# Kernel tuning notes

Hardware: AMD Instinct MI355X
Metric: run time of the kernel (lower is better)

Reference implementation:

```python
import jax, jax.numpy as jnp
import numpy as np


def _ste_round(r):
    # straight-through round
    return r + jax.lax.stop_gradient(jnp.round(r) - r)


def quant_sym(x, s, qn, qp):
    # symmetric LSQ-style fake-quant: clamp(round(x/s)) * s
    r = jnp.clip(x / s, qn, qp)
    return _ste_round(r) * s


def quant_asym(x, s, beta, qn, qp):
    # asymmetric fake-quant with learnable zero-point beta
    r = jnp.clip((x - beta) / s, qn, qp)
    return _ste_round(r) * s + beta


def quant_weight_statsq(w, n_bits=8):
    # statsq: per-output-channel scale from weight statistics
    qp = 2 ** (n_bits - 1) - 1          # 127
    qn = -(2 ** (n_bits - 1))           # -128
    s = 2.0 * jnp.mean(jnp.abs(w), axis=1, keepdims=True) / jnp.sqrt(float(qp))
    return quant_sym(w, s, qn, qp)


def setup_inputs() -> dict:
    key = jax.random.key(0)
    ks = jax.random.split(key, 8)
    B, N, C, H = 4, 4096, 1024, 4096
    x = jax.random.normal(ks[0], (B, N, C), dtype=jnp.float32)
    w1 = jax.random.normal(ks[1], (H, C), dtype=jnp.float32) * (1.0 / np.sqrt(C))
    b1 = jax.random.normal(ks[2], (H,), dtype=jnp.float32) * 0.01
    w2 = jax.random.normal(ks[3], (C, H), dtype=jnp.float32) * (1.0 / np.sqrt(H))
    b2 = jax.random.normal(ks[4], (C,), dtype=jnp.float32) * 0.01
    # learnable LSQ activation scales (per input channel), kept positive
    s_a1 = 0.05 + 0.05 * jax.random.uniform(ks[5], (C,), dtype=jnp.float32)
    s_a2 = 0.02 + 0.02 * jax.random.uniform(ks[6], (H,), dtype=jnp.float32)
    beta2 = jnp.zeros((H,), dtype=jnp.float32)
    return {"x": x, "w1": w1, "b1": b1, "w2": w2, "b2": b2,
            "s_a1": s_a1, "s_a2": s_a2, "beta2": beta2}


def reference(x, w1, b1, w2, b2, s_a1, s_a2, beta2):
    # fc1: symmetric 8-bit LSQ on input, statsq 8-bit on weight
    xq = quant_sym(x, s_a1, -128, 127)
    wq1 = quant_weight_statsq(w1)
    h = jnp.einsum('bnc,hc->bnh', xq, wq1) + b1
    h = jax.nn.gelu(h, approximate=False)  # nn.GELU default (exact erf)
    # drop1 = identity in eval
    # fc2: asymmetric 8-bit LSQ on (non-negative-skewed) activations
    hq = quant_asym(h, s_a2, beta2, 0, 255)
    wq2 = quant_weight_statsq(w2)
    out = jnp.einsum('bnh,ch->bnc', hq, wq2) + b2
    # drop2 = identity in eval
    return out
```

## Files before the change

kernel.cpp:

```cpp
#include <hip/hip_runtime.h>
#include <cstdint>
#include <cstddef>

typedef __attribute__((ext_vector_type(8))) short short8;
typedef __attribute__((ext_vector_type(4))) float f32x4;
typedef __attribute__((ext_vector_type(4))) unsigned short ushort4_t;

__device__ __forceinline__ unsigned short f2bf(float f) {
  unsigned u = __float_as_uint(f);
  u += 0x7FFFu + ((u >> 16) & 1u);
  return (unsigned short)(u >> 16);
}

__device__ __forceinline__ void gload_lds16(const void* g, void* lds) {
  __builtin_amdgcn_global_load_lds((const __attribute__((address_space(1))) void*)g,
                                   (__attribute__((address_space(3))) void*)lds,
                                   16, 0, 0);
}

__device__ __forceinline__ float erf_fast(float v) {
  float x = fabsf(v);
  float t = __builtin_amdgcn_rcpf(fmaf(0.3275911f, x, 1.0f));
  float p = fmaf(1.061405429f, t, -1.453152027f);
  p = fmaf(p, t, 1.421413741f);
  p = fmaf(p, t, -0.284496736f);
  p = fmaf(p, t, 0.254829592f);
  p = p * t;
  float e = fmaf(-p, __expf(-x * x), 1.0f);
  unsigned s = __float_as_uint(v) & 0x80000000u;
  return __uint_as_float(__float_as_uint(e) | s);
}

__global__ void quant_x_kernel(const float4* __restrict__ x, const float* __restrict__ s_a1,
                               ushort4_t* __restrict__ xq, int n4, int c4mask) {
  const int stride = gridDim.x * blockDim.x;
  for (int i = blockIdx.x * blockDim.x + threadIdx.x; i < n4; i += stride) {
    float4 v = x[i];
    int c = (i & c4mask) << 2;
    float vv[4] = {v.x, v.y, v.z, v.w};
    ushort4_t o;
#pragma unroll
    for (int j = 0; j < 4; ++j) {
      float s = s_a1[c + j];
      float r = vv[j] / s;
      r = fminf(fmaxf(r, -128.f), 127.f);
      o[j] = f2bf(rintf(r) * s);
    }
    xq[i] = o;
  }
}

__global__ void quant_w_kernel(const float* __restrict__ w, unsigned short* __restrict__ wq,
                               int cols) {
  const int row = blockIdx.x;
  const float* wr = w + (size_t)row * cols;
  float part = 0.f;
  for (int j = threadIdx.x; j < cols; j += blockDim.x) part += fabsf(wr[j]);
#pragma unroll
  for (int o = 32; o > 0; o >>= 1) part += __shfl_down(part, o, 64);
  __shared__ float wsum[4];
  if ((threadIdx.x & 63) == 0) wsum[threadIdx.x >> 6] = part;
  __syncthreads();
  float mean = (wsum[0] + wsum[1] + wsum[2] + wsum[3]) / (float)cols;
  float s = 2.f * mean / sqrtf(127.f);
  unsigned short* wqr = wq + (size_t)row * cols;
  for (int j = threadIdx.x; j < cols; j += blockDim.x) {
    float r = wr[j] / s;
    r = fminf(fmaxf(r, -128.f), 127.f);
    wqr[j] = f2bf(rintf(r) * s);
  }
}

#define BAR() __builtin_amdgcn_s_barrier()
#define SB() __builtin_amdgcn_sched_barrier(0)
#define LGKM(n) { asm volatile("s_waitcnt lgkmcnt(" #n ")" ::: "memory"); SB(); }
#define VMC0() { asm volatile("s_waitcnt vmcnt(0)" ::: "memory"); SB(); }
#define PRIO1() __builtin_amdgcn_s_setprio(1)
#define PRIO0() __builtin_amdgcn_s_setprio(0)

#define STG(gbase, ldsbuf, h, kt) { \
  _Pragma("unroll") for (int i_ = 0; i_ < 2; ++i_) { \
    const int rb_ = (h) * 128 + (w * 2 + i_) * 8; \
    gload_lds16((gbase) + (size_t)rb_ * K + (size_t)(kt) * 64, (void*)((ldsbuf) + rb_ * 64)); } }

#define LDA_(dst, buf, mh) { \
  _Pragma("unroll") for (int mi_ = 0; mi_ < 4; ++mi_) { \
    dst[mi_][0] = *(const short8*)((buf) + aBase + (mh) * 4096 + mi_ * 1024 + ck0); \
    dst[mi_][1] = *(const short8*)((buf) + aBase + (mh) * 4096 + mi_ * 1024 + ck1); } }

#define LDB_(dst, buf, nh) { \
  _Pragma("unroll") for (int ni_ = 0; ni_ < 2; ++ni_) { \
    dst[ni_][0] = *(const short8*)((buf) + bBase + (nh) * 2048 + ni_ * 1024 + ck0); \
    dst[ni_][1] = *(const short8*)((buf) + bBase + (nh) * 2048 + ni_ * 1024 + ck1); } }

#define MMQ(aR, bR, mh, nh) { \
  _Pragma("unroll") for (int kk_ = 0; kk_ < 2; ++kk_) \
  _Pragma("unroll") for (int mi_ = 0; mi_ < 4; ++mi_) \
  _Pragma("unroll") for (int ni_ = 0; ni_ < 2; ++ni_) \
    acc[(mh) * 4 + mi_][(nh) * 2 + ni_] = __builtin_amdgcn_mfma_f32_16x16x32_bf16( \
        aR[mi_][kk_], bR[ni_][kk_], acc[(mh) * 4 + mi_][(nh) * 2 + ni_], 0, 0, 0); }

template <int EPI>
__global__ __launch_bounds__(512, 2) void gemm_bt_pl(
    const unsigned short* __restrict__ A, const unsigned short* __restrict__ B,
    const float* __restrict__ bias, const float* __restrict__ s2,
    const float* __restrict__ beta, unsigned short* __restrict__ Cq,
    float* __restrict__ Cf, int N, int K)
{
  __shared__ __align__(16) unsigned short As0[256 * 64];
  __shared__ __align__(16) unsigned short As1[256 * 64];
  __shared__ __align__(16) unsigned short Bs0[256 * 64];
  __shared__ __align__(16) unsigned short Bs1[256 * 64];

  const int tid = threadIdx.x;
  const int w = tid >> 6, ll = tid & 63;
  const int wr = w >> 2, wc = w & 3;
  const long bm = (long)blockIdx.x * 256;
  const long bn = (long)blockIdx.y * 256;

  const int srow = ll >> 3;
  const int scol = ((ll & 7) ^ srow) << 3;
  const unsigned short* Agl = A + ((size_t)bm + srow) * K + scol;
  const unsigned short* Bgl = B + ((size_t)bn + srow) * K + scol;

  const int lhi = ll >> 4, llo = ll & 15, l7 = ll & 7;
  const int ck0 = ((0 * 4 + lhi) ^ l7) * 8;
  const int ck1 = ((1 * 4 + lhi) ^ l7) * 8;
  const int aBase = (wr * 128 + llo) * 64;
  const int bBase = (wc * 64 + llo) * 64;

  f32x4 acc[8][4] = {};
  short8 a0[4][2], a1[4][2], b0[2][2], b1[2][2];

  const int nkt = K >> 6;

  STG(Agl, As0, 0, 0); STG(Agl, As0, 1, 0);
  STG(Bgl, Bs0, 0, 0); STG(Bgl, Bs0, 1, 0);
  STG(Agl, As1, 0, 1); STG(Agl, As1, 1, 1);
  STG(Bgl, Bs1, 0, 1); STG(Bgl, Bs1, 1, 1);
  asm volatile("s_waitcnt vmcnt(8)" ::: "memory"); SB();
  BAR();
  LDA_(a0, As0, 0);
  LDB_(b0, Bs0, 0);

  for (int t = 0; t < nkt; ++t) {
    unsigned short* Asb = (t & 1) ? As1 : As0;
    unsigned short* Bsb = (t & 1) ? Bs1 : Bs0;
    unsigned short* Asn = (t & 1) ? As0 : As1;
    unsigned short* Bsn = (t & 1) ? Bs0 : Bs1;
    const bool i1 = (t + 1 < nkt), i2 = (t + 2 < nkt);

    LDB_(b1, Bsb, 1);
    LGKM(4);
    PRIO1(); MMQ(a0, b0, 0, 0); PRIO0();
    LDA_(a1, Asb, 1);
    LGKM(8);
    PRIO1(); MMQ(a0, b1, 0, 1); PRIO0();
    LGKM(0);
    PRIO1(); MMQ(a1, b0, 1, 0); PRIO0();
    VMC0();
    BAR();
    if (i2) {
      STG(Agl, Asb, 0, t + 2); STG(Agl, Asb, 1, t + 2);
      STG(Bgl, Bsb, 0, t + 2); STG(Bgl, Bsb, 1, t + 2);
    }
    if (i1) {
      LDA_(a0, Asn, 0);
      LDB_(b0, Bsn, 0);
    }
    PRIO1(); MMQ(a1, b1, 1, 1); PRIO0();
  }

  const int lr = lhi;
  const int lc = llo;
#pragma unroll
  for (int NI = 0; NI < 4; ++NI) {
    const long col = bn + wc * 64 + NI * 16 + lc;
    const float bv = bias[col];
    float sv = 1.f, bev = 0.f, inv = 1.f;
    if (EPI == 0) { sv = s2[col]; bev = beta[col]; inv = 1.0f / sv; }
#pragma unroll
    for (int MI = 0; MI < 8; ++MI) {
#pragma unroll
      for (int r = 0; r < 4; ++r) {
        const size_t rowg = (size_t)(bm + wr * 128 + MI * 16 + lr * 4 + r);
        float v = acc[MI][NI][r] + bv;
        if (EPI == 0) {
          float g = 0.5f * v * (1.f + erf_fast(v * 0.70710678118654752f));
          float rr = (g - bev) * inv;
          rr = fminf(fmaxf(rr, 0.f), 255.f);
          Cq[rowg * N + col] = f2bf(fmaf(rintf(rr), sv, bev));
        } else {
          Cf[rowg * N + col] = v;
        }
      }
    }
  }
}

extern "C" void kernel_launch(void* const* d_in, const int* in_sizes, int n_in,
                              void* d_out, int out_size, void* d_ws, size_t ws_size,
                              hipStream_t stream) {
  const float* x     = (const float*)d_in[0];
  const float* w1    = (const float*)d_in[1];
  const float* b1    = (const float*)d_in[2];
  const float* w2    = (const float*)d_in[3];
  const float* b2    = (const float*)d_in[4];
  const float* s_a1  = (const float*)d_in[5];
  const float* s_a2  = (const float*)d_in[6];
  const float* beta2 = (const float*)d_in[7];
  float* out = (float*)d_out;

  const int C = 1024, H = 4096;
  const int M = in_sizes[0] / C;

  unsigned short* xq  = (unsigned short*)d_ws;
  unsigned short* wq1 = xq  + (size_t)M * C;
  unsigned short* wq2 = wq1 + (size_t)H * C;
  unsigned short* hq  = wq2 + (size_t)C * H;

  quant_x_kernel<<<2048, 256, 0, stream>>>((const float4*)x, s_a1, (ushort4_t*)xq,
                                           M * C / 4, C / 4 - 1);
  quant_w_kernel<<<H, 256, 0, stream>>>(w1, wq1, C);
  quant_w_kernel<<<C, 256, 0, stream>>>(w2, wq2, H);

  dim3 g1(M / 256, H / 256);
  gemm_bt_pl<0><<<g1, 512, 0, stream>>>(xq, wq1, b1, s_a2, beta2, hq, nullptr, H, C);
  dim3 g2(M / 256, C / 256);
  gemm_bt_pl<1><<<g2, 512, 0, stream>>>(hq, wq2, b2, nullptr, nullptr, nullptr, out, C, H);
}
```

Measured before the change: 367.0 us.

## Unroll GEMM main loop by two with reordered LDS loads and MFMA ordering

Restructures the GEMM K-loop to process two k-tiles per iteration with fixed buffer addresses. Fragment loads are interleaved in a different order so MFMA quadrants reuse already-loaded A/B fragments, which aims to hide more LDS latency. The epilogue also hoists per-column bias and scale loads and reorders the stores by row. This assumes nkt is even, which holds for K=1024 and K=4096, and it increases code size.

```diff
diff --git a/kernel.cpp b/kernel.cpp
--- a/kernel.cpp
+++ b/kernel.cpp
@@ -101,7 +101,7 @@
         aR[mi_][kk_], bR[ni_][kk_], acc[(mh) * 4 + mi_][(nh) * 2 + ni_], 0, 0, 0); }
 
 template <int EPI>
-__global__ __launch_bounds__(512, 2) void gemm_bt_pl(
+__global__ __launch_bounds__(512, 2) void gemm_bt_gc(
     const unsigned short* __restrict__ A, const unsigned short* __restrict__ B,
     const float* __restrict__ bias, const float* __restrict__ s2,
     const float* __restrict__ beta, unsigned short* __restrict__ Cq,
@@ -130,7 +130,7 @@
   const int bBase = (wc * 64 + llo) * 64;
 
   f32x4 acc[8][4] = {};
-  short8 a0[4][2], a1[4][2], b0[2][2], b1[2][2];
+  short8 pa0[4][2], pa1[4][2], pb0[2][2], pb1[2][2];
 
   const int nkt = K >> 6;
 
@@ -139,59 +139,77 @@
   STG(Agl, As1, 0, 1); STG(Agl, As1, 1, 1);
   STG(Bgl, Bs1, 0, 1); STG(Bgl, Bs1, 1, 1);
   asm volatile("s_waitcnt vmcnt(8)" ::: "memory"); SB();
-  BAR();
-  LDA_(a0, As0, 0);
-  LDB_(b0, Bs0, 0);
-
-  for (int t = 0; t < nkt; ++t) {
-    unsigned short* Asb = (t & 1) ? As1 : As0;
-    unsigned short* Bsb = (t & 1) ? Bs1 : Bs0;
-    unsigned short* Asn = (t & 1) ? As0 : As1;
-    unsigned short* Bsn = (t & 1) ? Bs0 : Bs1;
-    const bool i1 = (t + 1 < nkt), i2 = (t + 2 < nkt);
-
-    LDB_(b1, Bsb, 1);
-    LGKM(4);
-    PRIO1(); MMQ(a0, b0, 0, 0); PRIO0();
-    LDA_(a1, Asb, 1);
-    LGKM(8);
-    PRIO1(); MMQ(a0, b1, 0, 1); PRIO0();
-    LGKM(0);
-    PRIO1(); MMQ(a1, b0, 1, 0); PRIO0();
-    VMC0();
-    BAR();
-    if (i2) {
-      STG(Agl, Asb, 0, t + 2); STG(Agl, Asb, 1, t + 2);
-      STG(Bgl, Bsb, 0, t + 2); STG(Bgl, Bsb, 1, t + 2);
-    }
-    if (i1) {
-      LDA_(a0, Asn, 0);
-      LDB_(b0, Bsn, 0);
-    }
-    PRIO1(); MMQ(a1, b1, 1, 1); PRIO0();
+  BAR(); SB();
+  LDB_(pb0, Bs0, 0);
+  LDA_(pa0, As0, 0);
+
+  for (int t = 0; t < nkt; t += 2) {
+    {
+      const bool s2a = (t + 2 < nkt);
+      LDA_(pa1, As0, 1);
+      LGKM(8);
+      PRIO1(); MMQ(pa0, pb0, 0, 0); PRIO0();
+      LDB_(pb1, Bs0, 1);
+      LGKM(4);
+      PRIO1(); MMQ(pa1, pb0, 1, 0); PRIO0();
+      LGKM(0);
+      VMC0();
+      BAR(); SB();
+      if (s2a) { STG(Agl, As0, 0, t + 2); STG(Agl, As0, 1, t + 2);
+                 STG(Bgl, Bs0, 0, t + 2); STG(Bgl, Bs0, 1, t + 2); }
+      LDB_(pb0, Bs1, 0);
+      PRIO1(); MMQ(pa1, pb1, 1, 1); PRIO0();
+      LDA_(pa1, As1, 1);
+      PRIO1(); MMQ(pa0, pb1, 0, 1); PRIO0();
+    }
+    {
+      const int to = t + 1;
+      const bool cont = (to + 1 < nkt);
+      const bool s3 = (to + 2 < nkt);
+      LDA_(pa0, As1, 0);
+      LGKM(8);
+      PRIO1(); MMQ(pa1, pb0, 1, 0); PRIO0();
+      LDB_(pb1, Bs1, 1);
+      LGKM(4);
+      PRIO1(); MMQ(pa0, pb0, 0, 0); PRIO0();
+      LGKM(0);
+      VMC0();
+      BAR(); SB();
+      if (s3) { STG(Agl, As1, 0, to + 2); STG(Agl, As1, 1, to + 2);
+                STG(Bgl, Bs1, 0, to + 2); STG(Bgl, Bs1, 1, to + 2); }
+      if (cont) LDB_(pb0, Bs0, 0);
+      PRIO1(); MMQ(pa0, pb1, 0, 1); PRIO0();
+      if (cont) LDA_(pa0, As0, 0);
+      PRIO1(); MMQ(pa1, pb1, 1, 1); PRIO0();
+    }
   }
 
   const int lr = lhi;
   const int lc = llo;
+  float bv[4], sv[4], bev[4], inv[4];
 #pragma unroll
   for (int NI = 0; NI < 4; ++NI) {
     const long col = bn + wc * 64 + NI * 16 + lc;
-    const float bv = bias[col];
-    float sv = 1.f, bev = 0.f, inv = 1.f;
-    if (EPI == 0) { sv = s2[col]; bev = beta[col]; inv = 1.0f / sv; }
-#pragma unroll
-    for (int MI = 0; MI < 8; ++MI) {
-#pragma unroll
-      for (int r = 0; r < 4; ++r) {
-        const size_t rowg = (size_t)(bm + wr * 128 + MI * 16 + lr * 4 + r);
-        float v = acc[MI][NI][r] + bv;
+    bv[NI] = bias[col];
+    if (EPI == 0) { sv[NI] = s2[col]; bev[NI] = beta[col]; inv[NI] = 1.0f / sv[NI]; }
+    else { sv[NI] = 1.f; bev[NI] = 0.f; inv[NI] = 1.f; }
+  }
+  const long colb = bn + wc * 64 + lc;
+#pragma unroll
+  for (int MI = 0; MI < 8; ++MI) {
+#pragma unroll
+    for (int r = 0; r < 4; ++r) {
+      const size_t rowg = (size_t)(bm + wr * 128 + MI * 16 + lr * 4 + r);
+#pragma unroll
+      for (int NI = 0; NI < 4; ++NI) {
+        float v = acc[MI][NI][r] + bv[NI];
         if (EPI == 0) {
           float g = 0.5f * v * (1.f + erf_fast(v * 0.70710678118654752f));
-          float rr = (g - bev) * inv;
+          float rr = (g - bev[NI]) * inv[NI];
           rr = fminf(fmaxf(rr, 0.f), 255.f);
-          Cq[rowg * N + col] = f2bf(fmaf(rintf(rr), sv, bev));
+          Cq[rowg * N + colb + NI * 16] = f2bf(fmaf(rintf(rr), sv[NI], bev[NI]));
         } else {
-          Cf[rowg * N + col] = v;
+          Cf[rowg * N + colb + NI * 16] = v;
         }
       }
     }
@@ -225,7 +243,7 @@
   quant_w_kernel<<<C, 256, 0, stream>>>(w2, wq2, H);
 
   dim3 g1(M / 256, H / 256);
-  gemm_bt_pl<0><<<g1, 512, 0, stream>>>(xq, wq1, b1, s_a2, beta2, hq, nullptr, H, C);
+  gemm_bt_gc<0><<<g1, 512, 0, stream>>>(xq, wq1, b1, s_a2, beta2, hq, nullptr, H, C);
   dim3 g2(M / 256, C / 256);
-  gemm_bt_pl<1><<<g2, 512, 0, stream>>>(hq, wq2, b2, nullptr, nullptr, nullptr, out, C, H);
-}
+  gemm_bt_gc<1><<<g2, 512, 0, stream>>>(hq, wq2, b2, nullptr, nullptr, nullptr, out, C, H);
+}
```

After: 521.8 us. +42.2%, slower.
